# Optimization experiments

Measured on AMD Instinct MI355X. Metric: run time of the kernel, lower is better.

Reference implementation:

```python
import jax, jax.numpy as jnp
import numpy as np

B, S = 16, 32768
LEVELS = (5, 20)
TIME_DIM = 8
NUM_FREQS = 6  # frequency xyz encoder: 3*(1+2*6)=39 dims
HID = 128
IN_DIM = 3 * (1 + 2 * NUM_FREQS) + 2 * TIME_DIM  # 55


def setup_inputs() -> dict:
    key = jax.random.key(0)
    ks = jax.random.split(key, 16)
    time = jax.random.uniform(ks[0], (B,), dtype=jnp.float32)
    xyz = jax.random.uniform(ks[1], (B, S, 3), dtype=jnp.float32) * 2.0 - 1.0  # in [-1,1]
    te0 = jax.random.normal(ks[2], (LEVELS[0] + 1, TIME_DIM), dtype=jnp.float32)
    te1 = jax.random.normal(ks[3], (LEVELS[1] + 1, TIME_DIM), dtype=jnp.float32)
    W0 = jax.random.normal(ks[4], (IN_DIM, HID), dtype=jnp.float32) * 0.05
    b0 = jnp.zeros((HID,), dtype=jnp.float32)
    W1 = jax.random.normal(ks[5], (HID, HID), dtype=jnp.float32) * 0.05
    b1 = jnp.zeros((HID,), dtype=jnp.float32)
    W2 = jax.random.normal(ks[6], (HID, HID), dtype=jnp.float32) * 0.05
    b2 = jnp.zeros((HID,), dtype=jnp.float32)
    Wout = jax.random.normal(ks[7], (HID, 1), dtype=jnp.float32) * 0.05
    bout = jnp.zeros((1,), dtype=jnp.float32)
    return {"time": time, "xyz": xyz, "te0": te0, "te1": te1,
            "W0": W0, "b0": b0, "W1": W1, "b1": b1, "W2": W2, "b2": b2,
            "Wout": Wout, "bout": bout}


def _time_encode(t, emb, L):
    # bucketize t into L uniform intervals on [0,1), lerp between bucket endpoints
    tL = t * L
    idx = jnp.clip(jnp.floor(tL).astype(jnp.int32), 0, L - 1)  # (B,)
    w = (idx + 1).astype(t.dtype) - tL                          # weight for lower endpoint
    lerped = w[:, None] * emb[idx] + (1.0 - w)[:, None] * emb[idx + 1]
    # t >= 1: use last embedding directly (torch fallback branch)
    return jnp.where((t >= 1.0)[:, None], emb[L][None, :], lerped)


def _xyz_encode(x):
    # frequency encoding, include_input, freqs 2^0..2^(NUM_FREQS-1)
    freqs = jnp.asarray(2.0 ** np.arange(NUM_FREQS), dtype=x.dtype)  # (F,)
    xp = x[:, None, :] * freqs[None, :, None]                         # (N, F, 3)
    n = x.shape[0]
    return jnp.concatenate([x, jnp.sin(xp).reshape(n, -1), jnp.cos(xp).reshape(n, -1)], axis=-1)


def reference(time, xyz, te0, te1, W0, b0, W1, b1, W2, b2, Wout, bout):
    s = xyz.shape[1]
    t_enc = jnp.concatenate([_time_encode(time, te0, LEVELS[0]),
                             _time_encode(time, te1, LEVELS[1])], axis=-1)  # (B, 16)
    t_enc = jnp.repeat(t_enc, s, axis=0)          # (B*S, 16)  'B d -> (B S) d'
    pts = (xyz.reshape(-1, 3) + 1.0) / 2.0        # (B*S, 3)
    x = jnp.concatenate([t_enc, _xyz_encode(pts)], axis=1)  # (B*S, 55)
    x = jax.nn.relu(x @ W0 + b0)
    x = jax.nn.relu(x @ W1 + b1)
    x = jax.nn.relu(x @ W2 + b2)
    return x @ Wout + bout  # (B*S, 1)
```

## Files before the change

### kernel.cpp

```cpp
#include <hip/hip_runtime.h>

typedef _Float16 f16;
typedef __attribute__((ext_vector_type(8))) _Float16 f16x8;
typedef __attribute__((ext_vector_type(4))) float f32x4;
typedef __attribute__((ext_vector_type(4))) unsigned int u32x4;

#define NPTS   (16 * 32768)
#define NTILES 1024
#define W0P_OFF 0
#define W1P_OFF (16 * 1024)
#define W2P_OFF (48 * 1024)
#define WOP_OFF (80 * 1024)
#define FRAGS_BYTES (84 * 1024)
#define TENC_OFF FRAGS_BYTES
#define WS_NEEDED (FRAGS_BYTES + 1024)
#define SCR_OFF FRAGS_BYTES
#define LDS_TOTAL (SCR_OFF + 8 * 8192)

__global__ void pack_weights(const float* __restrict__ time, const float* __restrict__ te0,
                             const float* __restrict__ te1, const float* __restrict__ W0,
                             const float* __restrict__ W1, const float* __restrict__ W2,
                             const float* __restrict__ Wout, unsigned char* __restrict__ ws) {
  const int bi = blockIdx.x;
  const int l = threadIdx.x;
  const int g = l >> 4, r16 = l & 15;
  if (bi < 84) {
    const float* W; int obase, fi, kt, mt, kmax; bool natural, outcol;
    if (bi < 16)      { W = W0;   fi = bi;      mt = fi >> 1; kt = fi & 1; obase = W0P_OFF; kmax = 55;  natural = true;  outcol = false; }
    else if (bi < 48) { W = W1;   fi = bi - 16; mt = fi >> 2; kt = fi & 3; obase = W1P_OFF; kmax = 128; natural = false; outcol = false; }
    else if (bi < 80) { W = W2;   fi = bi - 48; mt = fi >> 2; kt = fi & 3; obase = W2P_OFF; kmax = 128; natural = false; outcol = false; }
    else              { W = Wout; fi = bi - 80; mt = 0;       kt = fi;     obase = WOP_OFF; kmax = 128; natural = false; outcol = true;  }
    const int m = mt * 16 + r16;
    f16 vals[8] __attribute__((aligned(16)));
#pragma unroll
    for (int j = 0; j < 8; ++j) {
      const int k = natural ? (kt * 32 + g * 8 + j)
                            : (kt * 32 + (j >> 2) * 16 + g * 4 + (j & 3));
      float v = 0.f;
      if (k < kmax) v = outcol ? ((m == 0) ? Wout[k] : 0.f) : W[k * 128 + m];
      vals[j] = (f16)v;
    }
    *(u32x4*)(ws + obase + (fi * 64 + l) * 16) = *(const u32x4*)vals;
  } else {
    const int idx = (bi - 84) * 64 + l;
    const int b = idx >> 4, d = idx & 15;
    const float t = time[b];
    const float* emb; int L, dd;
    if (d < 8) { emb = te0; L = 5;  dd = d; }
    else       { emb = te1; L = 20; dd = d - 8; }
    const float tL = t * (float)L;
    int i = (int)floorf(tL);
    i = i < 0 ? 0 : (i > L - 1 ? L - 1 : i);
    const float wlo = (float)(i + 1) - tL;
    float v = wlo * emb[i * 8 + dd] + (1.f - wlo) * emb[(i + 1) * 8 + dd];
    if (t >= 1.f) v = emb[L * 8 + dd];
    ((float*)(ws + TENC_OFF))[idx] = v;
  }
}

template <int KT>
__device__ __forceinline__ void layer_swapped(const char* __restrict__ wlds,
                                              const float* __restrict__ bias,
                                              const f16x8 (&Bin)[KT][4], f16x8 (&Bout)[4][4],
                                              int lane) {
  const int g4 = (lane >> 4) * 4;
#pragma unroll
  for (int mtp = 0; mtp < 4; ++mtp) {
    const float4 ba = *(const float4*)(bias + mtp * 32 + g4);
    const float4 bb = *(const float4*)(bias + mtp * 32 + 16 + g4);
    f32x4 acc[2][4];
#pragma unroll
    for (int nt = 0; nt < 4; ++nt) {
      acc[0][nt] = (f32x4){ba.x, ba.y, ba.z, ba.w};
      acc[1][nt] = (f32x4){bb.x, bb.y, bb.z, bb.w};
    }
#pragma unroll
    for (int kt = 0; kt < KT; ++kt) {
      const f16x8 A0 = *(const f16x8*)(wlds + (((2 * mtp)     * KT + kt) * 64 + lane) * 16);
      const f16x8 A1 = *(const f16x8*)(wlds + (((2 * mtp + 1) * KT + kt) * 64 + lane) * 16);
#pragma unroll
      for (int nt = 0; nt < 4; ++nt)
        acc[0][nt] = __builtin_amdgcn_mfma_f32_16x16x32_f16(A0, Bin[kt][nt], acc[0][nt], 0, 0, 0);
#pragma unroll
      for (int nt = 0; nt < 4; ++nt)
        acc[1][nt] = __builtin_amdgcn_mfma_f32_16x16x32_f16(A1, Bin[kt][nt], acc[1][nt], 0, 0, 0);
    }
#pragma unroll
    for (int nt = 0; nt < 4; ++nt) {
      f16 tmp[8] __attribute__((aligned(16)));
#pragma unroll
      for (int r = 0; r < 4; ++r) {
        tmp[r]     = (f16)fmaxf(acc[0][nt][r], 0.f);
        tmp[4 + r] = (f16)fmaxf(acc[1][nt][r], 0.f);
      }
      Bout[mtp][nt] = *(const f16x8*)tmp;
    }
  }
}

__global__ void __launch_bounds__(512, 2)
mlp_main(const float* __restrict__ xyz, const float* __restrict__ b0,
         const float* __restrict__ b1, const float* __restrict__ b2,
         const float* __restrict__ bout, const unsigned char* __restrict__ ws,
         float* __restrict__ out) {
  extern __shared__ char lds[];
  const int tid = threadIdx.x;
  const int lane = tid & 63, wv = tid >> 6;
  const int g = lane >> 4, r16 = lane & 15;

  for (int i = tid; i < FRAGS_BYTES / 16; i += 512)
    *(u32x4*)(lds + i * 16) = *(const u32x4*)(ws + i * 16);
  __syncthreads();

  char* scr = lds + SCR_OFF + wv * 8192;
  const float bo = bout[0];

  for (int tile = blockIdx.x; tile < NTILES; tile += gridDim.x) {
    const int pbase = tile * 512 + wv * 64;
    const int p = pbase + lane;

    f16 feat[64] __attribute__((aligned(16)));
    const float* tb = (const float*)(ws + TENC_OFF) + (tile >> 6) * 16;
#pragma unroll
    for (int i = 0; i < 16; ++i) feat[i] = (f16)tb[i];
    const float xs0 = xyz[p * 3], xs1 = xyz[p * 3 + 1], xs2 = xyz[p * 3 + 2];
    const float pcs[3] = {(xs0 + 1.f) * 0.5f, (xs1 + 1.f) * 0.5f, (xs2 + 1.f) * 0.5f};
#pragma unroll
    for (int c = 0; c < 3; ++c) {
      feat[16 + c] = (f16)pcs[c];
      float s = __sinf(pcs[c]), co = __cosf(pcs[c]);
#pragma unroll
      for (int f = 0; f < 6; ++f) {
        feat[19 + f * 3 + c] = (f16)s;
        feat[37 + f * 3 + c] = (f16)co;
        const float s2 = 2.f * s * co, c2 = 1.f - 2.f * s * s;
        s = s2; co = c2;
      }
    }
#pragma unroll
    for (int i = 55; i < 64; ++i) feat[i] = (f16)0.f;

#pragma unroll
    for (int s = 0; s < 8; ++s)
      *(u32x4*)(scr + lane * 128 + ((s ^ (lane & 7)) * 16)) = ((const u32x4*)feat)[s];

    f16x8 B0[2][4];
#pragma unroll
    for (int kt = 0; kt < 2; ++kt)
#pragma unroll
      for (int nt = 0; nt < 4; ++nt) {
        const int row = nt * 16 + r16;
        B0[kt][nt] = *(const f16x8*)(scr + row * 128 + (((4 * kt + g) ^ (row & 7)) * 16));
      }

    f16x8 Bx[4][4], By[4][4];
    layer_swapped<2>((const char*)lds + W0P_OFF, b0, B0, Bx, lane);
    layer_swapped<4>((const char*)lds + W1P_OFF, b1, Bx, By, lane);
    layer_swapped<4>((const char*)lds + W2P_OFF, b2, By, Bx, lane);

    f32x4 accO[4];
#pragma unroll
    for (int nt = 0; nt < 4; ++nt) accO[nt] = (f32x4){bo, bo, bo, bo};
#pragma unroll
    for (int kt = 0; kt < 4; ++kt) {
      const f16x8 A = *(const f16x8*)((const char*)lds + WOP_OFF + (kt * 64 + lane) * 16);
#pragma unroll
      for (int nt = 0; nt < 4; ++nt)
        accO[nt] = __builtin_amdgcn_mfma_f32_16x16x32_f16(A, Bx[kt][nt], accO[nt], 0, 0, 0);
    }
    if (lane < 16) {
#pragma unroll
      for (int nt = 0; nt < 4; ++nt)
        out[pbase + nt * 16 + lane] = accO[nt][0];
    }
  }
}

extern "C" void kernel_launch(void* const* d_in, const int* in_sizes, int n_in,
                              void* d_out, int out_size, void* d_ws, size_t ws_size,
                              hipStream_t stream) {
  const float* time = (const float*)d_in[0];
  const float* xyz  = (const float*)d_in[1];
  const float* te0  = (const float*)d_in[2];
  const float* te1  = (const float*)d_in[3];
  const float* W0   = (const float*)d_in[4];
  const float* b0   = (const float*)d_in[5];
  const float* W1   = (const float*)d_in[6];
  const float* b1   = (const float*)d_in[7];
  const float* W2   = (const float*)d_in[8];
  const float* b2   = (const float*)d_in[9];
  const float* Wout = (const float*)d_in[10];
  const float* bout = (const float*)d_in[11];
  float* out = (float*)d_out;
  unsigned char* ws = (unsigned char*)d_ws;
  if (ws_size < WS_NEEDED) return;

  hipFuncSetAttribute((const void*)mlp_main,
                      hipFuncAttributeMaxDynamicSharedMemorySize, LDS_TOTAL);

  pack_weights<<<88, 64, 0, stream>>>(time, te0, te1, W0, W1, W2, Wout, ws);
  mlp_main<<<256, 512, LDS_TOTAL, stream>>>(xyz, b0, b1, b2, bout, ws, out);
}
```

Baseline: 52.81 us.

## Use 1024-thread blocks with halved scratch, setprio around MFMA, packed f16 converts

Doubles the block to 16 waves, each processing 1024 points per tile, and halves the per-wave feature scratch. The B0 fragments are now staged in two 32-lane halves. It adds s_setprio around the MFMA loops, replaces the scalar f16 conversions with cvt_pkrtz, and makes the output store fully coalesced through shuffles. The aim is more resident waves to hide latency. In exchange, launch_bounds(1024,4) forces a much smaller register budget, which risks spills. cvt_pkrtz also changes rounding to round-toward-zero.

```diff
diff --git a/kernel.cpp b/kernel.cpp
--- a/kernel.cpp
+++ b/kernel.cpp
@@ -1,12 +1,13 @@
 #include <hip/hip_runtime.h>
 
 typedef _Float16 f16;
+typedef __attribute__((ext_vector_type(2))) __fp16 fp16x2;
 typedef __attribute__((ext_vector_type(8))) _Float16 f16x8;
 typedef __attribute__((ext_vector_type(4))) float f32x4;
 typedef __attribute__((ext_vector_type(4))) unsigned int u32x4;
 
 #define NPTS   (16 * 32768)
-#define NTILES 1024
+#define NTILES 512
 #define W0P_OFF 0
 #define W1P_OFF (16 * 1024)
 #define W2P_OFF (48 * 1024)
@@ -15,7 +16,7 @@
 #define TENC_OFF FRAGS_BYTES
 #define WS_NEEDED (FRAGS_BYTES + 1024)
 #define SCR_OFF FRAGS_BYTES
-#define LDS_TOTAL (SCR_OFF + 8 * 8192)
+#define LDS_TOTAL (SCR_OFF + 16 * 4096)
 
 __global__ void pack_weights(const float* __restrict__ time, const float* __restrict__ te0,
                              const float* __restrict__ te1, const float* __restrict__ W0,
@@ -74,6 +75,7 @@
       acc[0][nt] = (f32x4){ba.x, ba.y, ba.z, ba.w};
       acc[1][nt] = (f32x4){bb.x, bb.y, bb.z, bb.w};
     }
+    __builtin_amdgcn_s_setprio(1);
 #pragma unroll
     for (int kt = 0; kt < KT; ++kt) {
       const f16x8 A0 = *(const f16x8*)(wlds + (((2 * mtp)     * KT + kt) * 64 + lane) * 16);
@@ -85,20 +87,20 @@
       for (int nt = 0; nt < 4; ++nt)
         acc[1][nt] = __builtin_amdgcn_mfma_f32_16x16x32_f16(A1, Bin[kt][nt], acc[1][nt], 0, 0, 0);
     }
+    __builtin_amdgcn_s_setprio(0);
 #pragma unroll
     for (int nt = 0; nt < 4; ++nt) {
-      f16 tmp[8] __attribute__((aligned(16)));
-#pragma unroll
-      for (int r = 0; r < 4; ++r) {
-        tmp[r]     = (f16)fmaxf(acc[0][nt][r], 0.f);
-        tmp[4 + r] = (f16)fmaxf(acc[1][nt][r], 0.f);
-      }
-      Bout[mtp][nt] = *(const f16x8*)tmp;
+      union { fp16x2 h2[4]; f16x8 v; } u;
+      u.h2[0] = __builtin_amdgcn_cvt_pkrtz(fmaxf(acc[0][nt][0], 0.f), fmaxf(acc[0][nt][1], 0.f));
+      u.h2[1] = __builtin_amdgcn_cvt_pkrtz(fmaxf(acc[0][nt][2], 0.f), fmaxf(acc[0][nt][3], 0.f));
+      u.h2[2] = __builtin_amdgcn_cvt_pkrtz(fmaxf(acc[1][nt][0], 0.f), fmaxf(acc[1][nt][1], 0.f));
+      u.h2[3] = __builtin_amdgcn_cvt_pkrtz(fmaxf(acc[1][nt][2], 0.f), fmaxf(acc[1][nt][3], 0.f));
+      Bout[mtp][nt] = u.v;
     }
   }
 }
 
-__global__ void __launch_bounds__(512, 2)
+__global__ void __launch_bounds__(1024, 4)
 mlp_main(const float* __restrict__ xyz, const float* __restrict__ b0,
          const float* __restrict__ b1, const float* __restrict__ b2,
          const float* __restrict__ bout, const unsigned char* __restrict__ ws,
@@ -108,19 +110,19 @@
   const int lane = tid & 63, wv = tid >> 6;
   const int g = lane >> 4, r16 = lane & 15;
 
-  for (int i = tid; i < FRAGS_BYTES / 16; i += 512)
+  for (int i = tid; i < FRAGS_BYTES / 16; i += 1024)
     *(u32x4*)(lds + i * 16) = *(const u32x4*)(ws + i * 16);
   __syncthreads();
 
-  char* scr = lds + SCR_OFF + wv * 8192;
+  char* scr = lds + SCR_OFF + wv * 4096;
   const float bo = bout[0];
 
   for (int tile = blockIdx.x; tile < NTILES; tile += gridDim.x) {
-    const int pbase = tile * 512 + wv * 64;
+    const int pbase = tile * 1024 + wv * 64;
     const int p = pbase + lane;
 
     f16 feat[64] __attribute__((aligned(16)));
-    const float* tb = (const float*)(ws + TENC_OFF) + (tile >> 6) * 16;
+    const float* tb = (const float*)(ws + TENC_OFF) + (tile >> 5) * 16;
 #pragma unroll
     for (int i = 0; i < 16; ++i) feat[i] = (f16)tb[i];
     const float xs0 = xyz[p * 3], xs1 = xyz[p * 3 + 1], xs2 = xyz[p * 3 + 2];
@@ -140,18 +142,24 @@
 #pragma unroll
     for (int i = 55; i < 64; ++i) feat[i] = (f16)0.f;
 
-#pragma unroll
-    for (int s = 0; s < 8; ++s)
-      *(u32x4*)(scr + lane * 128 + ((s ^ (lane & 7)) * 16)) = ((const u32x4*)feat)[s];
-
     f16x8 B0[2][4];
 #pragma unroll
-    for (int kt = 0; kt < 2; ++kt)
-#pragma unroll
-      for (int nt = 0; nt < 4; ++nt) {
-        const int row = nt * 16 + r16;
-        B0[kt][nt] = *(const f16x8*)(scr + row * 128 + (((4 * kt + g) ^ (row & 7)) * 16));
+    for (int h = 0; h < 2; ++h) {
+      if ((lane >> 5) == h) {
+#pragma unroll
+        for (int s = 0; s < 8; ++s)
+          *(u32x4*)(scr + (lane & 31) * 128 + ((s ^ (lane & 7)) * 16)) = ((const u32x4*)feat)[s];
       }
+      asm volatile("s_waitcnt lgkmcnt(0)" ::: "memory");
+#pragma unroll
+      for (int kt = 0; kt < 2; ++kt)
+#pragma unroll
+        for (int nn = 0; nn < 2; ++nn) {
+          const int row = nn * 16 + r16;
+          B0[kt][h * 2 + nn] = *(const f16x8*)(scr + row * 128 + (((4 * kt + g) ^ (row & 7)) * 16));
+        }
+      asm volatile("s_waitcnt lgkmcnt(0)" ::: "memory");
+    }
 
     f16x8 Bx[4][4], By[4][4];
     layer_swapped<2>((const char*)lds + W0P_OFF, b0, B0, Bx, lane);
@@ -161,6 +169,7 @@
     f32x4 accO[4];
 #pragma unroll
     for (int nt = 0; nt < 4; ++nt) accO[nt] = (f32x4){bo, bo, bo, bo};
+    __builtin_amdgcn_s_setprio(1);
 #pragma unroll
     for (int kt = 0; kt < 4; ++kt) {
       const f16x8 A = *(const f16x8*)((const char*)lds + WOP_OFF + (kt * 64 + lane) * 16);
@@ -168,11 +177,14 @@
       for (int nt = 0; nt < 4; ++nt)
         accO[nt] = __builtin_amdgcn_mfma_f32_16x16x32_f16(A, Bx[kt][nt], accO[nt], 0, 0, 0);
     }
-    if (lane < 16) {
-#pragma unroll
-      for (int nt = 0; nt < 4; ++nt)
-        out[pbase + nt * 16 + lane] = accO[nt][0];
-    }
+    __builtin_amdgcn_s_setprio(0);
+
+    const float a0 = __shfl(accO[0][0], r16, 64);
+    const float a1 = __shfl(accO[1][0], r16, 64);
+    const float a2 = __shfl(accO[2][0], r16, 64);
+    const float a3 = __shfl(accO[3][0], r16, 64);
+    const float v = g == 0 ? a0 : g == 1 ? a1 : g == 2 ? a2 : a3;
+    out[pbase + lane] = v;
   }
 }
 
@@ -199,5 +211,5 @@
                       hipFuncAttributeMaxDynamicSharedMemorySize, LDS_TOTAL);
 
   pack_weights<<<88, 64, 0, stream>>>(time, te0, te1, W0, W1, W2, Wout, ws);
-  mlp_main<<<256, 512, LDS_TOTAL, stream>>>(xyz, b0, b1, b2, bout, ws, out);
-}
+  mlp_main<<<256, 1024, LDS_TOTAL, stream>>>(xyz, b0, b1, b2, bout, ws, out);
+}
```

Measured after the change: 69.45 us. +31.5%, slower.
